# Performance work log

Hardware: AMD Instinct MI355X
Metric: run time of the kernel (lower is better)

The kernel has to match this reference:

```python
import jax, jax.numpy as jnp
import numpy as np

B, S, E, H = 4, 1024, 1024, 16
HD = E // H  # 64


def setup_inputs() -> dict:
    key = jax.random.key(0)
    ks = jax.random.split(key, 9)
    scale = 1.0 / np.sqrt(E)
    x = jax.random.normal(ks[0], (B, S, E), dtype=jnp.float32)
    attention_mask = jnp.ones((B, S, S), dtype=jnp.int32)
    # per-head projection weights, batched over heads: [H, E, HD]
    Wq = jax.random.normal(ks[1], (H, E, HD), dtype=jnp.float32) * scale
    Wk = jax.random.normal(ks[2], (H, E, HD), dtype=jnp.float32) * scale
    Wv = jax.random.normal(ks[3], (H, E, HD), dtype=jnp.float32) * scale
    bq = jax.random.normal(ks[4], (H, HD), dtype=jnp.float32) * scale
    bk = jax.random.normal(ks[5], (H, HD), dtype=jnp.float32) * scale
    bv = jax.random.normal(ks[6], (H, HD), dtype=jnp.float32) * scale
    # output projection, torch Linear convention: [out_features, in_features]
    Wo = jax.random.normal(ks[7], (E, E), dtype=jnp.float32) * scale
    bo = jax.random.normal(ks[8], (E,), dtype=jnp.float32) * scale
    return {"x": x, "attention_mask": attention_mask, "Wq": Wq, "bq": bq,
            "Wk": Wk, "bk": bk, "Wv": Wv, "bv": bv, "Wo": Wo, "bo": bo}


def reference(x, attention_mask, Wq, bq, Wk, bk, Wv, bv, Wo, bo):
    # batched-over-heads QKV projections: (B,S,E) x (H,E,HD) -> (B,H,S,HD)
    q = jnp.einsum('bse,hed->bhsd', x, Wq) + bq[None, :, None, :]
    k = jnp.einsum('bse,hed->bhsd', x, Wk) + bk[None, :, None, :]
    v = jnp.einsum('bse,hed->bhsd', x, Wv) + bv[None, :, None, :]
    scores = jnp.einsum('bhsd,bhtd->bhst', q, k) / jnp.sqrt(jnp.float32(HD))
    mask = attention_mask[:, None, :, :]  # (B,1,S,S) broadcast over heads
    scores = jnp.where(mask == 0, -jnp.inf, scores)
    weights = jax.nn.softmax(scores, axis=-1)
    out = jnp.einsum('bhst,bhtd->bhsd', weights, v)
    # concat heads on last dim: (B,S,H*HD) == (B,S,E)
    out = out.transpose(0, 2, 1, 3).reshape(B, S, E)
    return out @ Wo.T + bo
```

## Files before the change

### kernel.cpp

```cpp
#include <hip/hip_runtime.h>
#include <hip/hip_bf16.h>

#define NB 4
#define SEQ 1024
#define EMB 1024
#define NH 16
#define HD 64

typedef unsigned short u16;
typedef __attribute__((ext_vector_type(8))) __bf16 bf16x8;
typedef __attribute__((ext_vector_type(8))) short short8;
typedef __attribute__((ext_vector_type(4))) float floatx4;

__device__ inline u16 f2b_rn(float f) {
    union { float f; unsigned int i; } x; x.f = f;
    unsigned int r = (x.i + 0x7FFFu + ((x.i >> 16) & 1u)) >> 16;
    return (u16)r;
}
__device__ inline bf16x8 s2b(short8 v) {
    union { short8 s; bf16x8 b; } x; x.s = v; return x.b;
}

__device__ inline void gload_lds16(const void* g, void* l) {
    __builtin_amdgcn_global_load_lds(
        (const __attribute__((address_space(1))) void*)g,
        (__attribute__((address_space(3))) void*)l, 16, 0, 0);
}

__device__ inline bf16x8 ldsfrag(const u16* base, int r, int c) {
    return s2b(*(const short8*)&base[r * 64 + (c ^ ((r & 7) * 8))]);
}

__device__ inline void cvt8(const float* __restrict__ s, u16* __restrict__ d) {
    float4 a = *(const float4*)(s);
    float4 b = *(const float4*)(s + 4);
    union { u16 u[8]; int4 v; } o;
    o.u[0] = f2b_rn(a.x); o.u[1] = f2b_rn(a.y); o.u[2] = f2b_rn(a.z); o.u[3] = f2b_rn(a.w);
    o.u[4] = f2b_rn(b.x); o.u[5] = f2b_rn(b.y); o.u[6] = f2b_rn(b.z); o.u[7] = f2b_rn(b.w);
    *(int4*)(d) = o.v;
}

__global__ __launch_bounds__(256) void prep(
    const float* __restrict__ x, const float* __restrict__ Wq,
    const float* __restrict__ Wk, const float* __restrict__ Wv,
    const float* __restrict__ Wo, const int* __restrict__ mask,
    u16* __restrict__ xb, u16* __restrict__ Wt, u16* __restrict__ Wob,
    unsigned long long* __restrict__ bits)
{
    __shared__ u16 T[64 * 80];
    int bx = blockIdx.x;
    int tid = threadIdx.x;

    if (bx < 2048) {
        int i = bx * 2048 + tid * 8;
        cvt8(x + i, xb + i);
    } else if (bx < 2560) {
        int i = (bx - 2048) * 2048 + tid * 8;
        cvt8(Wo + i, Wob + i);
    } else if (bx < 3328) {
        int bx2 = bx - 2560;
        int e0 = (bx2 & 15) * 64;
        int ph = bx2 >> 4;
        int p = ph >> 4, h = ph & 15;
        const float* W = (p == 0 ? Wq : (p == 1 ? Wk : Wv)) + h * (EMB * HD);
        #pragma unroll
        for (int c = 0; c < 2; ++c) {
            int flat = c * 2048 + tid * 8;
            int r = flat >> 6;
            int d = flat & 63;
            cvt8(W + (size_t)(e0 + r) * HD + d, &T[r * 80 + d]);
        }
        __syncthreads();
        int d = tid >> 2;
        int ec = tid & 3;
        union { u16 u[16]; int4 v[2]; } tmp;
        #pragma unroll
        for (int i = 0; i < 16; ++i) tmp.u[i] = T[(ec * 16 + i) * 80 + d];
        u16* dst = Wt + ((size_t)(p * NH + h) * HD + d) * EMB + e0 + ec * 16;
        *(int4*)(dst) = tmp.v[0];
        *(int4*)(dst + 8) = tmp.v[1];
    } else {
        int gw = (bx - 3328) * 4 + (tid >> 6);
        int lane = tid & 63;
        int m = mask[(size_t)gw * 64 + lane];
        unsigned long long bl = __ballot(m != 0);
        if (lane == 0) bits[gw] = bl;
    }
}

__global__ __launch_bounds__(256) void qkv_gemm(
    const u16* __restrict__ x,
    const u16* __restrict__ Wt2,
    const float* __restrict__ bq, const float* __restrict__ bk, const float* __restrict__ bv,
    u16* __restrict__ Q, u16* __restrict__ K, u16* __restrict__ Vt)
{
    __shared__ u16 As[128 * 64];
    __shared__ u16 Bs[128 * 64];

    int m0 = blockIdx.x * 128;
    int n0 = blockIdx.y * 128;
    int tid = threadIdx.x;
    int w = tid >> 6, lane = tid & 63, quad = lane >> 4, ln = lane & 15;
    int wm = w & 1, wn = w >> 1;

    floatx4 acc[4][4] = {};

    for (int k0 = 0; k0 < EMB; k0 += 64) {
        __syncthreads();
        #pragma unroll
        for (int i = 0; i < 4; ++i) {
            int flat0 = i * 256 + (tid & 192);
            int flat = flat0 + lane;
            int r = flat >> 3;
            int c = ((flat & 7) ^ (r & 7)) * 8;
            gload_lds16(x   + (size_t)(m0 + r) * EMB + k0 + c, As + flat0 * 8);
            gload_lds16(Wt2 + (size_t)(n0 + r) * EMB + k0 + c, Bs + flat0 * 8);
        }
        __syncthreads();

        #pragma unroll
        for (int kk = 0; kk < 2; ++kk) {
            bf16x8 a[4], bf[4];
            #pragma unroll
            for (int mt = 0; mt < 4; ++mt)
                a[mt] = ldsfrag(As, wm * 64 + mt * 16 + ln, kk * 32 + quad * 8);
            #pragma unroll
            for (int nc = 0; nc < 4; ++nc)
                bf[nc] = ldsfrag(Bs, wn * 64 + nc * 16 + ln, kk * 32 + quad * 8);
            #pragma unroll
            for (int mt = 0; mt < 4; ++mt)
                #pragma unroll
                for (int nc = 0; nc < 4; ++nc)
                    acc[mt][nc] = __builtin_amdgcn_mfma_f32_16x16x32_bf16(a[mt], bf[nc], acc[mt][nc], 0, 0, 0);
        }
    }

    int p = n0 >> 10;
    const float* bias = (p == 0 ? bq : (p == 1 ? bk : bv));
    if (p < 2) {
        u16* Out = (p == 0) ? Q : K;
        float qs = (p == 0) ? 0.125f * 1.44269504f : 1.0f;
        #pragma unroll
        for (int nc = 0; nc < 4; ++nc) {
            int n = n0 + wn * 64 + nc * 16 + ln;
            int h = (n >> 6) & 15, d = n & 63;
            float bv_ = bias[n & 1023];
            #pragma unroll
            for (int mt = 0; mt < 4; ++mt) {
                #pragma unroll
                for (int reg = 0; reg < 4; ++reg) {
                    int m = m0 + wm * 64 + mt * 16 + quad * 4 + reg;
                    int b_ = m >> 10, s = m & 1023;
                    Out[((size_t)(b_ * NH + h) * SEQ + s) * HD + d] = f2b_rn((acc[mt][nc][reg] + bv_) * qs);
                }
            }
        }
    } else {
        #pragma unroll
        for (int nc = 0; nc < 4; ++nc) {
            int n = n0 + wn * 64 + nc * 16 + ln;
            int h = (n >> 6) & 15, d = n & 63;
            float bv_ = bias[n & 1023];
            #pragma unroll
            for (int mt = 0; mt < 4; ++mt) {
                int m = m0 + wm * 64 + mt * 16 + quad * 4;
                int b_ = m >> 10, s = m & 1023;
                union { u16 u[4]; uint2 v; } pk;
                #pragma unroll
                for (int reg = 0; reg < 4; ++reg)
                    pk.u[reg] = f2b_rn(acc[mt][nc][reg] + bv_);
                *(uint2*)&Vt[((size_t)(b_ * NH + h) * HD + d) * SEQ + s] = pk.v;
            }
        }
    }
}

__global__ __launch_bounds__(128) void attn(
    const u16* __restrict__ Q, const u16* __restrict__ K, const u16* __restrict__ Vt,
    const unsigned long long* __restrict__ bits,
    u16* __restrict__ Aout)
{
    const int PP = 72;
    __shared__ u16 Ks[64 * 64];
    __shared__ u16 Vs[80 * 64];
    __shared__ u16 Ps[64 * PP];

    int q0 = blockIdx.x * 64;
    int bh = blockIdx.y;
    int b = bh >> 4, h = bh & 15;
    const u16* Qb = Q  + (size_t)bh * SEQ * HD;
    const u16* Kb = K  + (size_t)bh * SEQ * HD;
    const u16* Vb = Vt + (size_t)bh * HD * SEQ;

    int tid = threadIdx.x;
    int w = tid >> 6, lane = tid & 63, quad = lane >> 4, ln = lane & 15;

    if (tid < 16) *(uint2*)&Vs[64 * 64 + tid * 4] = make_uint2(0x3F803F80u, 0x3F803F80u);

    bf16x8 qf[2][2];
    #pragma unroll
    for (int s = 0; s < 2; ++s) {
        const u16* qp = Qb + (size_t)(q0 + w * 32 + s * 16 + ln) * HD + quad * 8;
        union { int4 i; bf16x8 b; } c0, c1;
        c0.i = *(const int4*)(qp);
        c1.i = *(const int4*)(qp + 32);
        qf[s][0] = c0.b; qf[s][1] = c1.b;
    }

    floatx4 o[2][5] = {};

    for (int tt = 0; tt < SEQ / 64; ++tt) {
        int t0 = tt * 64;
        __syncthreads();
        #pragma unroll
        for (int i = 0; i < 4; ++i) {
            int flat0 = i * 128 + (tid & 64);
            int flat = flat0 + lane;
            int r = flat >> 3;
            int c = ((flat & 7) ^ (r & 7)) * 8;
            gload_lds16(Kb + (size_t)(t0 + r) * HD + c, Ks + flat0 * 8);
            gload_lds16(Vb + (size_t)r * SEQ + t0 + c, Vs + flat0 * 8);
        }
        __syncthreads();

        floatx4 sc[2][4] = {};
        #pragma unroll
        for (int kk = 0; kk < 2; ++kk) {
            bf16x8 kf[4];
            #pragma unroll
            for (int tb = 0; tb < 4; ++tb)
                kf[tb] = ldsfrag(Ks, tb * 16 + ln, kk * 32 + quad * 8);
            #pragma unroll
            for (int s = 0; s < 2; ++s)
                #pragma unroll
                for (int tb = 0; tb < 4; ++tb)
                    sc[s][tb] = __builtin_amdgcn_mfma_f32_16x16x32_bf16(kf[tb], qf[s][kk], sc[s][tb], 0, 0, 0);
        }

        #pragma unroll
        for (int s = 0; s < 2; ++s) {
            unsigned long long bm = bits[((size_t)b * SEQ + q0 + w * 32 + s * 16 + ln) * 16 + tt];
            if (__any(bm != ~0ull)) {
                #pragma unroll
                for (int tb = 0; tb < 4; ++tb)
                    #pragma unroll
                    for (int reg = 0; reg < 4; ++reg)
                        if (!((bm >> (tb * 16 + quad * 4 + reg)) & 1)) sc[s][tb][reg] = -1e30f;
            }
        }

        #pragma unroll
        for (int s = 0; s < 2; ++s) {
            int mrow = w * 32 + s * 16 + ln;
            #pragma unroll
            for (int tb = 0; tb < 4; ++tb) {
                union { float f; unsigned int i; } e0_, e1_, e2_, e3_;
                e0_.f = __builtin_amdgcn_exp2f(sc[s][tb][0]);
                e1_.f = __builtin_amdgcn_exp2f(sc[s][tb][1]);
                e2_.f = __builtin_amdgcn_exp2f(sc[s][tb][2]);
                e3_.f = __builtin_amdgcn_exp2f(sc[s][tb][3]);
                uint2 pk;
                pk.x = ((e0_.i + 0x8000u) >> 16) | ((e1_.i + 0x8000u) & 0xFFFF0000u);
                pk.y = ((e2_.i + 0x8000u) >> 16) | ((e3_.i + 0x8000u) & 0xFFFF0000u);
                *(uint2*)&Ps[mrow * PP + tb * 16 + quad * 4] = pk;
            }
        }

        #pragma unroll
        for (int kk = 0; kk < 2; ++kk) {
            bf16x8 vf[5];
            #pragma unroll
            for (int dt = 0; dt < 5; ++dt)
                vf[dt] = ldsfrag(Vs, dt * 16 + ln, kk * 32 + quad * 8);
            #pragma unroll
            for (int s = 0; s < 2; ++s) {
                bf16x8 pf = s2b(*(const short8*)&Ps[(w * 32 + s * 16 + ln) * PP + kk * 32 + quad * 8]);
                #pragma unroll
                for (int dt = 0; dt < 5; ++dt)
                    o[s][dt] = __builtin_amdgcn_mfma_f32_16x16x32_bf16(pf, vf[dt], o[s][dt], 0, 0, 0);
            }
        }
    }

    #pragma unroll
    for (int s = 0; s < 2; ++s) {
        #pragma unroll
        for (int reg = 0; reg < 4; ++reg) {
            float l = __shfl(o[s][4][reg], lane & 48, 64);
            float inv = 1.0f / l;
            int m = q0 + w * 32 + s * 16 + quad * 4 + reg;
            #pragma unroll
            for (int dt = 0; dt < 4; ++dt)
                Aout[((size_t)b * SEQ + m) * EMB + h * HD + dt * 16 + ln] = f2b_rn(o[s][dt][reg] * inv);
        }
    }
}

__global__ __launch_bounds__(256) void out_proj(
    const u16* __restrict__ A,
    const u16* __restrict__ Wo,
    const float* __restrict__ bo,
    float* __restrict__ Out)
{
    __shared__ u16 As[128 * 64];
    __shared__ u16 Bs[128 * 64];

    int m0 = blockIdx.x * 128;
    int n0 = blockIdx.y * 128;
    int tid = threadIdx.x;
    int w = tid >> 6, lane = tid & 63, quad = lane >> 4, ln = lane & 15;
    int wm = w & 1, wn = w >> 1;

    floatx4 acc[4][4] = {};

    for (int k0 = 0; k0 < EMB; k0 += 64) {
        __syncthreads();
        #pragma unroll
        for (int i = 0; i < 4; ++i) {
            int flat0 = i * 256 + (tid & 192);
            int flat = flat0 + lane;
            int r = flat >> 3;
            int c = ((flat & 7) ^ (r & 7)) * 8;
            gload_lds16(A  + (size_t)(m0 + r) * EMB + k0 + c, As + flat0 * 8);
            gload_lds16(Wo + (size_t)(n0 + r) * EMB + k0 + c, Bs + flat0 * 8);
        }
        __syncthreads();

        #pragma unroll
        for (int kk = 0; kk < 2; ++kk) {
            bf16x8 a[4], bf[4];
            #pragma unroll
            for (int mt = 0; mt < 4; ++mt)
                a[mt] = ldsfrag(As, wm * 64 + mt * 16 + ln, kk * 32 + quad * 8);
            #pragma unroll
            for (int nc = 0; nc < 4; ++nc)
                bf[nc] = ldsfrag(Bs, wn * 64 + nc * 16 + ln, kk * 32 + quad * 8);
            #pragma unroll
            for (int mt = 0; mt < 4; ++mt)
                #pragma unroll
                for (int nc = 0; nc < 4; ++nc)
                    acc[mt][nc] = __builtin_amdgcn_mfma_f32_16x16x32_bf16(a[mt], bf[nc], acc[mt][nc], 0, 0, 0);
        }
    }

    #pragma unroll
    for (int nc = 0; nc < 4; ++nc) {
        int n = n0 + wn * 64 + nc * 16 + ln;
        float bb = bo[n];
        #pragma unroll
        for (int mt = 0; mt < 4; ++mt) {
            #pragma unroll
            for (int reg = 0; reg < 4; ++reg) {
                int m = m0 + wm * 64 + mt * 16 + quad * 4 + reg;
                Out[(size_t)m * EMB + n] = acc[mt][nc][reg] + bb;
            }
        }
    }
}

extern "C" void kernel_launch(void* const* d_in, const int* in_sizes, int n_in,
                              void* d_out, int out_size, void* d_ws, size_t ws_size,
                              hipStream_t stream) {
    const float* x  = (const float*)d_in[0];
    const int*   mk = (const int*)d_in[1];
    const float* Wq = (const float*)d_in[2];
    const float* bq = (const float*)d_in[3];
    const float* Wk = (const float*)d_in[4];
    const float* bk = (const float*)d_in[5];
    const float* Wv = (const float*)d_in[6];
    const float* bv = (const float*)d_in[7];
    const float* Wo = (const float*)d_in[8];
    const float* bo = (const float*)d_in[9];
    float* out = (float*)d_out;

    const size_t MB = 1u << 20;
    char* ws = (char*)d_ws;
    u16* xb  = (u16*)ws;
    u16* Wt  = (u16*)(ws + 8 * MB);
    u16* Wob = (u16*)(ws + 14 * MB);
    unsigned long long* bits = (unsigned long long*)(ws + 16 * MB);
    u16* Qw  = (u16*)(ws + 16 * MB + 512 * 1024);
    u16* Kw  = (u16*)(ws + 24 * MB + 512 * 1024);
    u16* Vtw = (u16*)(ws + 32 * MB + 512 * 1024);
    u16* Ao  = xb;

    prep<<<19712, 256, 0, stream>>>(x, Wq, Wk, Wv, Wo, mk, xb, Wt, Wob, bits);
    qkv_gemm<<<dim3((NB * SEQ) / 128, 3 * EMB / 128), 256, 0, stream>>>(
        xb, Wt, bq, bk, bv, Qw, Kw, Vtw);
    attn<<<dim3(SEQ / 64, NB * NH), 128, 0, stream>>>(Qw, Kw, Vtw, bits, Ao);
    out_proj<<<dim3((NB * SEQ) / 128, EMB / 128), 256, 0, stream>>>(Ao, Wob, bo, out);
}
```

Before: 207.7 us.

## Double-buffer LDS in QKV and output GEMMs, halve out_proj M tile

```diff
diff --git a/kernel.cpp b/kernel.cpp
--- a/kernel.cpp
+++ b/kernel.cpp
@@ -29,6 +29,9 @@
 
 __device__ inline bf16x8 ldsfrag(const u16* base, int r, int c) {
     return s2b(*(const short8*)&base[r * 64 + (c ^ ((r & 7) * 8))]);
+}
+__device__ inline bf16x8 ldsfrag32(const u16* base, int r, int c) {
+    return s2b(*(const short8*)&base[r * 32 + (c ^ ((r & 3) * 8))]);
 }
 
 __device__ inline void cvt8(const float* __restrict__ s, u16* __restrict__ d) {
@@ -94,8 +97,8 @@
     const float* __restrict__ bq, const float* __restrict__ bk, const float* __restrict__ bv,
     u16* __restrict__ Q, u16* __restrict__ K, u16* __restrict__ Vt)
 {
-    __shared__ u16 As[128 * 64];
-    __shared__ u16 Bs[128 * 64];
+    __shared__ u16 As[2][128 * 32];
+    __shared__ u16 Bs[2][128 * 32];
 
     int m0 = blockIdx.x * 128;
     int n0 = blockIdx.y * 128;
@@ -105,34 +108,36 @@
 
     floatx4 acc[4][4] = {};
 
-    for (int k0 = 0; k0 < EMB; k0 += 64) {
-        __syncthreads();
-        #pragma unroll
-        for (int i = 0; i < 4; ++i) {
+    auto stage = [&](int k0, int buf) {
+        #pragma unroll
+        for (int i = 0; i < 2; ++i) {
             int flat0 = i * 256 + (tid & 192);
             int flat = flat0 + lane;
-            int r = flat >> 3;
-            int c = ((flat & 7) ^ (r & 7)) * 8;
-            gload_lds16(x   + (size_t)(m0 + r) * EMB + k0 + c, As + flat0 * 8);
-            gload_lds16(Wt2 + (size_t)(n0 + r) * EMB + k0 + c, Bs + flat0 * 8);
-        }
+            int r = flat >> 2;
+            int c = ((flat & 3) ^ (r & 3)) * 8;
+            gload_lds16(x   + (size_t)(m0 + r) * EMB + k0 + c, &As[buf][flat0 * 8]);
+            gload_lds16(Wt2 + (size_t)(n0 + r) * EMB + k0 + c, &Bs[buf][flat0 * 8]);
+        }
+    };
+
+    stage(0, 0);
+    for (int it = 0; it < 32; ++it) {
         __syncthreads();
-
-        #pragma unroll
-        for (int kk = 0; kk < 2; ++kk) {
-            bf16x8 a[4], bf[4];
-            #pragma unroll
-            for (int mt = 0; mt < 4; ++mt)
-                a[mt] = ldsfrag(As, wm * 64 + mt * 16 + ln, kk * 32 + quad * 8);
+        if (it < 31) stage((it + 1) * 32, (it + 1) & 1);
+        const u16* Ab = As[it & 1];
+        const u16* Bb = Bs[it & 1];
+        bf16x8 a[4], bfr[4];
+        #pragma unroll
+        for (int mt = 0; mt < 4; ++mt)
+            a[mt] = ldsfrag32(Ab, wm * 64 + mt * 16 + ln, quad * 8);
+        #pragma unroll
+        for (int nc = 0; nc < 4; ++nc)
+            bfr[nc] = ldsfrag32(Bb, wn * 64 + nc * 16 + ln, quad * 8);
+        #pragma unroll
+        for (int mt = 0; mt < 4; ++mt)
             #pragma unroll
             for (int nc = 0; nc < 4; ++nc)
-                bf[nc] = ldsfrag(Bs, wn * 64 + nc * 16 + ln, kk * 32 + quad * 8);
-            #pragma unroll
-            for (int mt = 0; mt < 4; ++mt)
-                #pragma unroll
-                for (int nc = 0; nc < 4; ++nc)
-                    acc[mt][nc] = __builtin_amdgcn_mfma_f32_16x16x32_bf16(a[mt], bf[nc], acc[mt][nc], 0, 0, 0);
-        }
+                acc[mt][nc] = __builtin_amdgcn_mfma_f32_16x16x32_bf16(a[mt], bfr[nc], acc[mt][nc], 0, 0, 0);
     }
 
     int p = n0 >> 10;
@@ -302,45 +307,53 @@
     const float* __restrict__ bo,
     float* __restrict__ Out)
 {
-    __shared__ u16 As[128 * 64];
-    __shared__ u16 Bs[128 * 64];
-
-    int m0 = blockIdx.x * 128;
+    __shared__ u16 As[2][64 * 32];
+    __shared__ u16 Bs[2][128 * 32];
+
+    int m0 = blockIdx.x * 64;
     int n0 = blockIdx.y * 128;
     int tid = threadIdx.x;
     int w = tid >> 6, lane = tid & 63, quad = lane >> 4, ln = lane & 15;
     int wm = w & 1, wn = w >> 1;
 
-    floatx4 acc[4][4] = {};
-
-    for (int k0 = 0; k0 < EMB; k0 += 64) {
-        __syncthreads();
-        #pragma unroll
-        for (int i = 0; i < 4; ++i) {
+    floatx4 acc[2][4] = {};
+
+    auto stage = [&](int k0, int buf) {
+        {
+            int flat0 = (tid & 192);
+            int flat = flat0 + lane;
+            int r = flat >> 2;
+            int c = ((flat & 3) ^ (r & 3)) * 8;
+            gload_lds16(A + (size_t)(m0 + r) * EMB + k0 + c, &As[buf][flat0 * 8]);
+        }
+        #pragma unroll
+        for (int i = 0; i < 2; ++i) {
             int flat0 = i * 256 + (tid & 192);
             int flat = flat0 + lane;
-            int r = flat >> 3;
-            int c = ((flat & 7) ^ (r & 7)) * 8;
-            gload_lds16(A  + (size_t)(m0 + r) * EMB + k0 + c, As + flat0 * 8);
-            gload_lds16(Wo + (size_t)(n0 + r) * EMB + k0 + c, Bs + flat0 * 8);
-        }
+            int r = flat >> 2;
+            int c = ((flat & 3) ^ (r & 3)) * 8;
+            gload_lds16(Wo + (size_t)(n0 + r) * EMB + k0 + c, &Bs[buf][flat0 * 8]);
+        }
+    };
+
+    stage(0, 0);
+    for (int it = 0; it < 32; ++it) {
         __syncthreads();
-
-        #pragma unroll
-        for (int kk = 0; kk < 2; ++kk) {
-            bf16x8 a[4], bf[4];
-            #pragma unroll
-            for (int mt = 0; mt < 4; ++mt)
-                a[mt] = ldsfrag(As, wm * 64 + mt * 16 + ln, kk * 32 + quad * 8);
+        if (it < 31) stage((it + 1) * 32, (it + 1) & 1);
+        const u16* Ab = As[it & 1];
+        const u16* Bb = Bs[it & 1];
+        bf16x8 a[2], bfr[4];
+        #pragma unroll
+        for (int mt = 0; mt < 2; ++mt)
+            a[mt] = ldsfrag32(Ab, wm * 32 + mt * 16 + ln, quad * 8);
+        #pragma unroll
+        for (int nc = 0; nc < 4; ++nc)
+            bfr[nc] = ldsfrag32(Bb, wn * 64 + nc * 16 + ln, quad * 8);
+        #pragma unroll
+        for (int mt = 0; mt < 2; ++mt)
             #pragma unroll
             for (int nc = 0; nc < 4; ++nc)
-                bf[nc] = ldsfrag(Bs, wn * 64 + nc * 16 + ln, kk * 32 + quad * 8);
-            #pragma unroll
-            for (int mt = 0; mt < 4; ++mt)
-                #pragma unroll
-                for (int nc = 0; nc < 4; ++nc)
-                    acc[mt][nc] = __builtin_amdgcn_mfma_f32_16x16x32_bf16(a[mt], bf[nc], acc[mt][nc], 0, 0, 0);
-        }
+                acc[mt][nc] = __builtin_amdgcn_mfma_f32_16x16x32_bf16(a[mt], bfr[nc], acc[mt][nc], 0, 0, 0);
     }
 
     #pragma unroll
@@ -348,10 +361,10 @@
         int n = n0 + wn * 64 + nc * 16 + ln;
         float bb = bo[n];
         #pragma unroll
-        for (int mt = 0; mt < 4; ++mt) {
+        for (int mt = 0; mt < 2; ++mt) {
             #pragma unroll
             for (int reg = 0; reg < 4; ++reg) {
-                int m = m0 + wm * 64 + mt * 16 + quad * 4 + reg;
+                int m = m0 + wm * 32 + mt * 16 + quad * 4 + reg;
                 Out[(size_t)m * EMB + n] = acc[mt][nc][reg] + bb;
             }
         }
@@ -388,5 +401,5 @@
     qkv_gemm<<<dim3((NB * SEQ) / 128, 3 * EMB / 128), 256, 0, stream>>>(
         xb, Wt, bq, bk, bv, Qw, Kw, Vtw);
     attn<<<dim3(SEQ / 64, NB * NH), 128, 0, stream>>>(Qw, Kw, Vtw, bits, Ao);
-    out_proj<<<dim3((NB * SEQ) / 128, EMB / 128), 256, 0, stream>>>(Ao, Wob, bo, out);
-}
+    out_proj<<<dim3((NB * SEQ) / 64, EMB / 128), 256, 0, stream>>>(Ao, Wob, bo, out);
+}
```

After: 215.5 us. +3.8%, slower.

## Overlap Wo conversion and mask packing with QKV GEMM; shrink out_proj M tile

Applied to the files above, without the earlier changes.

```diff
diff --git a/kernel.cpp b/kernel.cpp
--- a/kernel.cpp
+++ b/kernel.cpp
@@ -43,9 +43,7 @@
 __global__ __launch_bounds__(256) void prep(
     const float* __restrict__ x, const float* __restrict__ Wq,
     const float* __restrict__ Wk, const float* __restrict__ Wv,
-    const float* __restrict__ Wo, const int* __restrict__ mask,
-    u16* __restrict__ xb, u16* __restrict__ Wt, u16* __restrict__ Wob,
-    unsigned long long* __restrict__ bits)
+    u16* __restrict__ xb, u16* __restrict__ Wt)
 {
     __shared__ u16 T[64 * 80];
     int bx = blockIdx.x;
@@ -54,11 +52,8 @@
     if (bx < 2048) {
         int i = bx * 2048 + tid * 8;
         cvt8(x + i, xb + i);
-    } else if (bx < 2560) {
-        int i = (bx - 2048) * 2048 + tid * 8;
-        cvt8(Wo + i, Wob + i);
-    } else if (bx < 3328) {
-        int bx2 = bx - 2560;
+    } else {
+        int bx2 = bx - 2048;
         int e0 = (bx2 & 15) * 64;
         int ph = bx2 >> 4;
         int p = ph >> 4, h = ph & 15;
@@ -79,12 +74,6 @@
         u16* dst = Wt + ((size_t)(p * NH + h) * HD + d) * EMB + e0 + ec * 16;
         *(int4*)(dst) = tmp.v[0];
         *(int4*)(dst + 8) = tmp.v[1];
-    } else {
-        int gw = (bx - 3328) * 4 + (tid >> 6);
-        int lane = tid & 63;
-        int m = mask[(size_t)gw * 64 + lane];
-        unsigned long long bl = __ballot(m != 0);
-        if (lane == 0) bits[gw] = bl;
     }
 }
 
@@ -92,14 +81,35 @@
     const u16* __restrict__ x,
     const u16* __restrict__ Wt2,
     const float* __restrict__ bq, const float* __restrict__ bk, const float* __restrict__ bv,
-    u16* __restrict__ Q, u16* __restrict__ K, u16* __restrict__ Vt)
+    const float* __restrict__ Wo, const int* __restrict__ mask,
+    u16* __restrict__ Q, u16* __restrict__ K, u16* __restrict__ Vt,
+    u16* __restrict__ Wob, unsigned long long* __restrict__ bits)
 {
     __shared__ u16 As[128 * 64];
     __shared__ u16 Bs[128 * 64];
 
-    int m0 = blockIdx.x * 128;
-    int n0 = blockIdx.y * 128;
+    int gid = blockIdx.x;
     int tid = threadIdx.x;
+
+    if (gid >= 768) {
+        if (gid < 1280) {
+            int i = (gid - 768) * 2048 + tid * 8;
+            cvt8(Wo + i, Wob + i);
+        } else {
+            int base = (gid - 1280) * 256 + (tid >> 6) * 64;
+            int lane = tid & 63;
+            for (int i = 0; i < 64; ++i) {
+                int gw = base + i;
+                int m = mask[(size_t)gw * 64 + lane];
+                unsigned long long bl = __ballot(m != 0);
+                if (lane == 0) bits[gw] = bl;
+            }
+        }
+        return;
+    }
+
+    int m0 = (gid & 31) * 128;
+    int n0 = (gid >> 5) * 128;
     int w = tid >> 6, lane = tid & 63, quad = lane >> 4, ln = lane & 15;
     int wm = w & 1, wn = w >> 1;
 
@@ -302,44 +312,51 @@
     const float* __restrict__ bo,
     float* __restrict__ Out)
 {
-    __shared__ u16 As[128 * 64];
+    __shared__ u16 As[64 * 64];
     __shared__ u16 Bs[128 * 64];
 
-    int m0 = blockIdx.x * 128;
+    int m0 = blockIdx.x * 64;
     int n0 = blockIdx.y * 128;
     int tid = threadIdx.x;
     int w = tid >> 6, lane = tid & 63, quad = lane >> 4, ln = lane & 15;
     int wm = w & 1, wn = w >> 1;
 
-    floatx4 acc[4][4] = {};
+    floatx4 acc[2][4] = {};
 
     for (int k0 = 0; k0 < EMB; k0 += 64) {
         __syncthreads();
+        #pragma unroll
+        for (int i = 0; i < 2; ++i) {
+            int flat0 = i * 256 + (tid & 192);
+            int flat = flat0 + lane;
+            int r = flat >> 3;
+            int c = ((flat & 7) ^ (r & 7)) * 8;
+            gload_lds16(A + (size_t)(m0 + r) * EMB + k0 + c, As + flat0 * 8);
+        }
         #pragma unroll
         for (int i = 0; i < 4; ++i) {
             int flat0 = i * 256 + (tid & 192);
             int flat = flat0 + lane;
             int r = flat >> 3;
             int c = ((flat & 7) ^ (r & 7)) * 8;
-            gload_lds16(A  + (size_t)(m0 + r) * EMB + k0 + c, As + flat0 * 8);
             gload_lds16(Wo + (size_t)(n0 + r) * EMB + k0 + c, Bs + flat0 * 8);
         }
         __syncthreads();
 
         #pragma unroll
         for (int kk = 0; kk < 2; ++kk) {
-            bf16x8 a[4], bf[4];
-            #pragma unroll
-            for (int mt = 0; mt < 4; ++mt)
-                a[mt] = ldsfrag(As, wm * 64 + mt * 16 + ln, kk * 32 + quad * 8);
+            bf16x8 a[2], bfr[4];
+            #pragma unroll
+            for (int mt = 0; mt < 2; ++mt)
+                a[mt] = ldsfrag(As, wm * 32 + mt * 16 + ln, kk * 32 + quad * 8);
             #pragma unroll
             for (int nc = 0; nc < 4; ++nc)
-                bf[nc] = ldsfrag(Bs, wn * 64 + nc * 16 + ln, kk * 32 + quad * 8);
-            #pragma unroll
-            for (int mt = 0; mt < 4; ++mt)
+                bfr[nc] = ldsfrag(Bs, wn * 64 + nc * 16 + ln, kk * 32 + quad * 8);
+            #pragma unroll
+            for (int mt = 0; mt < 2; ++mt)
                 #pragma unroll
                 for (int nc = 0; nc < 4; ++nc)
-                    acc[mt][nc] = __builtin_amdgcn_mfma_f32_16x16x32_bf16(a[mt], bf[nc], acc[mt][nc], 0, 0, 0);
+                    acc[mt][nc] = __builtin_amdgcn_mfma_f32_16x16x32_bf16(a[mt], bfr[nc], acc[mt][nc], 0, 0, 0);
         }
     }
 
@@ -348,10 +365,10 @@
         int n = n0 + wn * 64 + nc * 16 + ln;
         float bb = bo[n];
         #pragma unroll
-        for (int mt = 0; mt < 4; ++mt) {
+        for (int mt = 0; mt < 2; ++mt) {
             #pragma unroll
             for (int reg = 0; reg < 4; ++reg) {
-                int m = m0 + wm * 64 + mt * 16 + quad * 4 + reg;
+                int m = m0 + wm * 32 + mt * 16 + quad * 4 + reg;
                 Out[(size_t)m * EMB + n] = acc[mt][nc][reg] + bb;
             }
         }
@@ -384,9 +401,9 @@
     u16* Vtw = (u16*)(ws + 32 * MB + 512 * 1024);
     u16* Ao  = xb;
 
-    prep<<<19712, 256, 0, stream>>>(x, Wq, Wk, Wv, Wo, mk, xb, Wt, Wob, bits);
-    qkv_gemm<<<dim3((NB * SEQ) / 128, 3 * EMB / 128), 256, 0, stream>>>(
-        xb, Wt, bq, bk, bv, Qw, Kw, Vtw);
+    prep<<<2816, 256, 0, stream>>>(x, Wq, Wk, Wv, xb, Wt);
+    qkv_gemm<<<1536, 256, 0, stream>>>(
+        xb, Wt, bq, bk, bv, Wo, mk, Qw, Kw, Vtw, Wob, bits);
     attn<<<dim3(SEQ / 64, NB * NH), 128, 0, stream>>>(Qw, Kw, Vtw, bits, Ao);
-    out_proj<<<dim3((NB * SEQ) / 128, EMB / 128), 256, 0, stream>>>(Ao, Wob, bo, out);
-}
+    out_proj<<<dim3((NB * SEQ) / 64, EMB / 128), 256, 0, stream>>>(Ao, Wob, bo, out);
+}
```

Result: no change. 211.5 us (+1.8%).
